# Kernel tuning notes

Measured on AMD Instinct MI355X. Metric: run time of the kernel, lower is better.

The kernel has to match this reference:

```python
import jax, jax.numpy as jnp
import numpy as np


def setup_inputs() -> dict:
    key = jax.random.key(0)
    ks = jax.random.split(key, 8)
    B, C, H, W = 16, 192, 64, 64
    dt_rank, d_state = 12, 1
    return {
        "x": jax.random.normal(ks[0], (B, C, H, W), dtype=jnp.float32),
        "conv_w": jax.random.normal(ks[1], (C, 1, 5, 5), dtype=jnp.float32) * 0.1,
        "conv_b": jax.random.normal(ks[2], (C,), dtype=jnp.float32) * 0.1,
        "x_proj_w": jax.random.normal(ks[3], (dt_rank + 2 * d_state, C), dtype=jnp.float32) * (C ** -0.5),
        "dt_w": jax.random.normal(ks[4], (C, dt_rank), dtype=jnp.float32) * (dt_rank ** -0.5),
        "dt_b": jax.random.normal(ks[5], (C,), dtype=jnp.float32) * 0.1,
        "A_logs": jnp.zeros((C, d_state), dtype=jnp.float32),  # log(arange(1,d_state+1)) with d_state=1 -> 0
        "Ds": jnp.ones((C,), dtype=jnp.float32),
    }


def reference(x, conv_w, conv_b, x_proj_w, dt_w, dt_b, A_logs, Ds):
    B, C, H, W = x.shape
    L = H * W
    dt_rank = dt_w.shape[1]
    n = A_logs.shape[1]  # d_state
    # depthwise conv2d, kernel 5, padding SAME (=d_conv//2), then SiLU
    x = jax.lax.conv_general_dilated(
        x, conv_w, window_strides=(1, 1), padding='SAME',
        feature_group_count=C, dimension_numbers=('NCHW', 'OIHW', 'NCHW'))
    x = jax.nn.silu(x + conv_b[None, :, None, None])
    xs = x.reshape(B, C, L)  # (b, d, l)
    # x_proj: (dt_rank + 2n, C) @ (b, C, l)
    x_dbl = jnp.einsum('kc,bcl->bkl', x_proj_w, xs)
    dts, Bs, Cs = jnp.split(x_dbl, [dt_rank, dt_rank + n], axis=1)
    # dt projection + softplus (delta_softplus=True with delta_bias)
    delta = jax.nn.softplus(jnp.einsum('cr,brl->bcl', dt_w, dts) + dt_b[None, :, None])  # (b,d,l)
    A = -jnp.exp(A_logs)  # (d, n)
    # selective scan returning the full state trajectory h_t (b,d,n,l):
    # h_t = exp(delta_t * A) * h_{t-1} + delta_t * B_t * u_t
    a = jnp.exp(delta[:, :, None, :] * A[None, :, :, None])        # (b,d,n,l)
    b_el = delta[:, :, None, :] * Bs[:, None, :, :] * xs[:, :, None, :]  # (b,d,n,l)

    def combine(e1, e2):
        a1, b1 = e1
        a2, b2 = e2
        return (a1 * a2, a2 * b1 + b2)

    _, h = jax.lax.associative_scan(combine, (a, b_el), axis=-1)  # h: (b,d,n,l)
    state = h.reshape(B, C * n, L)
    # y = C_t * h_t + D * u (fp32, d_state=1 broadcast)
    y = state.astype(jnp.float32) * Cs.astype(jnp.float32) + xs * Ds[:, None]
    return y.reshape(B, C, H, W)
```

## Files before the change

kernel.cpp:

```cpp
#include <hip/hip_runtime.h>
#include <hip/hip_bf16.h>
#include <cstddef>

#define BB 16
#define CC 192
#define HH 64
#define WW 64
#define LL 4096
#define DTR 12
#define KK 14

__device__ __forceinline__ float silu_f(float v) {
  return v / (1.f + __expf(-v));
}

__global__ __launch_bounds__(256) void conv_silu_kernel(
    const float* __restrict__ x, const float* __restrict__ cw,
    const float* __restrict__ cb, float* __restrict__ xs) {
  const int bc = blockIdx.x;
  const int c = bc % CC;
  const int tid = threadIdx.x;
  const int lane = tid & 63;
  const int wv = tid >> 6;
  const int oy0 = wv * 16;

  float w[25];
#pragma unroll
  for (int k = 0; k < 25; ++k) w[k] = cw[c * 25 + k];
  const float bias = cb[c];

  const float* xp = x + (size_t)bc * LL + lane;
  float* op = xs + (size_t)bc * LL + lane;

  float rv[20];
#pragma unroll
  for (int r = 0; r < 20; ++r) {
    const int gr = oy0 + r - 2;
    float v = 0.f;
    if ((unsigned)gr < 64u) v = xp[gr * 64];
    rv[r] = v;
  }

  float acc[5];
#pragma unroll
  for (int i = 0; i < 5; ++i) acc[i] = 0.f;

#pragma unroll
  for (int r = 0; r < 20; ++r) {
    float v = rv[r];
    float vm2 = __shfl_up(v, 2u, 64);
    float vm1 = __shfl_up(v, 1u, 64);
    float vp1 = __shfl_down(v, 1u, 64);
    float vp2 = __shfl_down(v, 2u, 64);
    if (lane < 2) vm2 = 0.f;
    if (lane < 1) vm1 = 0.f;
    if (lane > 62) vp1 = 0.f;
    if (lane > 61) vp2 = 0.f;
    float t[5] = {vm2, vm1, v, vp1, vp2};
#pragma unroll
    for (int ky = 0; ky < 5; ++ky) {
      if (r >= ky && (r - ky) < 16) {
        float s = acc[(r - ky) % 5];
#pragma unroll
        for (int kx = 0; kx < 5; ++kx) s += w[ky * 5 + kx] * t[kx];
        acc[(r - ky) % 5] = s;
      }
    }
    if (r >= 4) {
      const int yf = oy0 + r - 4;
      float a = acc[(r - 4) % 5] + bias;
      op[yf * 64] = silu_f(a);
      acc[(r - 4) % 5] = 0.f;
    }
  }
}

__global__ __launch_bounds__(512) void proj_kernel(
    const float* __restrict__ xs, const float* __restrict__ xpw,
    float* __restrict__ xdbl) {
  const int b = blockIdx.y;
  const int l0 = blockIdx.x * 128;
  const int tid = threadIdx.x;
  const int lane = tid & 63;
  const int g = tid >> 6;

  __shared__ float part[8][KK][132];

  float2 acc[KK];
#pragma unroll
  for (int k = 0; k < KK; ++k) acc[k] = make_float2(0.f, 0.f);

  const float* bp = xs + ((size_t)(b * CC + g * 24)) * LL + l0 + lane * 2;
#pragma unroll 4
  for (int cc = 0; cc < 24; ++cc) {
    float2 v = *(const float2*)(bp + (size_t)cc * LL);
    const int c = g * 24 + cc;
#pragma unroll
    for (int k = 0; k < KK; ++k) {
      float wv = xpw[k * CC + c];
      acc[k].x += wv * v.x;
      acc[k].y += wv * v.y;
    }
  }
#pragma unroll
  for (int k = 0; k < KK; ++k)
    *(float2*)&part[g][k][lane * 2] = acc[k];
  __syncthreads();

  for (int idx = tid; idx < KK * 128; idx += 512) {
    int k = idx >> 7, ln = idx & 127;
    float v = 0.f;
#pragma unroll
    for (int p = 0; p < 8; ++p) v += part[p][k][ln];
    xdbl[((size_t)b * KK + k) * LL + l0 + ln] = v;
  }
}

__global__ __launch_bounds__(64) void scan_kernel(
    const float* __restrict__ xs, const float* __restrict__ xdbl,
    const float* __restrict__ dtw, const float* __restrict__ dtb,
    const float* __restrict__ A_logs, const float* __restrict__ Ds,
    float* __restrict__ y) {
  const int bc = blockIdx.x;
  const int b = bc / CC;
  const int c = bc - b * CC;
  const int lane = threadIdx.x;

  const float Ac = -__expf(A_logs[c]);
  const float Dc = Ds[c];
  float dw[DTR];
#pragma unroll
  for (int r = 0; r < DTR; ++r) dw[r] = dtw[c * DTR + r];
  const float db = dtb[c];

  const float* xp = xs + (size_t)bc * LL;
  const float* xb = xdbl + (size_t)b * KK * LL;
  float* yp = y + (size_t)bc * LL;

  float hcarry = 0.f;

  auto load_chunk = [&](int sc, float4* dst) {
    const int base = sc * 256 + lane * 4;
    dst[0] = *(const float4*)(xp + base);
    dst[1] = *(const float4*)(xb + 12 * LL + base);
    dst[2] = *(const float4*)(xb + 13 * LL + base);
#pragma unroll
    for (int r = 0; r < DTR; ++r)
      dst[3 + r] = *(const float4*)(xb + r * LL + base);
  };

  auto process = [&](int sc, const float4* buf) {
    const int base = sc * 256 + lane * 4;
    const float4 x4 = buf[0];
    const float4 B4 = buf[1];
    const float4 C4 = buf[2];
    float xx[4] = {x4.x, x4.y, x4.z, x4.w};
    float bb[4] = {B4.x, B4.y, B4.z, B4.w};
    float av[4], bv[4];
    float aggA = 1.f, aggB = 0.f;
#pragma unroll
    for (int q = 0; q < 4; ++q) {
      float z = db;
#pragma unroll
      for (int r = 0; r < DTR; ++r) z += dw[r] * ((&buf[3 + r].x)[q]);
      float delta = (z > 15.f) ? z : __logf(1.f + __expf(z));
      float a = __expf(delta * Ac);
      float be = delta * bb[q] * xx[q];
      av[q] = a;
      bv[q] = be;
      aggA = a * aggA;
      aggB = a * aggB + be;
    }

    float incA = aggA, incB = aggB;
#pragma unroll
    for (int s = 1; s < 64; s <<= 1) {
      float pA = __shfl_up(incA, (unsigned)s, 64);
      float pB = __shfl_up(incB, (unsigned)s, 64);
      if (lane >= s) {
        incB = incA * pB + incB;
        incA = incA * pA;
      }
    }
    float eA = __shfl_up(incA, 1u, 64);
    float eB = __shfl_up(incB, 1u, 64);
    if (lane == 0) { eA = 1.f; eB = 0.f; }
    float tA = __shfl(incA, 63, 64);
    float tB = __shfl(incB, 63, 64);

    float h = eA * hcarry + eB;
    float ov[4];
#pragma unroll
    for (int q = 0; q < 4; ++q) {
      h = av[q] * h + bv[q];
      ov[q] = h * ((&C4.x)[q]) + xx[q] * Dc;
    }
    float4 o;
    o.x = ov[0]; o.y = ov[1]; o.z = ov[2]; o.w = ov[3];
    *(float4*)(yp + base) = o;

    hcarry = tA * hcarry + tB;
  };

  float4 bufA[15], bufB[15];
  load_chunk(0, bufA);
  for (int i = 0; i < 8; ++i) {
    const int s0 = 2 * i;
    load_chunk(s0 + 1, bufB);
    process(s0, bufA);
    load_chunk(s0 + 2 < 16 ? s0 + 2 : 15, bufA);
    process(s0 + 1, bufB);
  }
}

extern "C" void kernel_launch(void* const* d_in, const int* in_sizes, int n_in,
                              void* d_out, int out_size, void* d_ws,
                              size_t ws_size, hipStream_t stream) {
  const float* x        = (const float*)d_in[0];
  const float* conv_w   = (const float*)d_in[1];
  const float* conv_b   = (const float*)d_in[2];
  const float* x_proj_w = (const float*)d_in[3];
  const float* dt_w     = (const float*)d_in[4];
  const float* dt_b     = (const float*)d_in[5];
  const float* A_logs   = (const float*)d_in[6];
  const float* Ds       = (const float*)d_in[7];
  float* out = (float*)d_out;

  char* ws = (char*)d_ws;
  const size_t plane_bytes = (size_t)BB * CC * LL * sizeof(float);
  float* xs   = (float*)ws;
  float* xdbl = (float*)(ws + plane_bytes);

  conv_silu_kernel<<<dim3(BB * CC), 256, 0, stream>>>(x, conv_w, conv_b, xs);
  proj_kernel<<<dim3(LL / 128, BB), 512, 0, stream>>>(xs, x_proj_w, xdbl);
  scan_kernel<<<dim3(BB * CC), 64, 0, stream>>>(xs, xdbl, dt_w, dt_b,
                                                A_logs, Ds, out);
}
```

Before: 167.9 us.

## Split scan sequence across four wavefronts with cross-segment carry fixup

The scan kernel now uses 256 threads per (batch, channel) block, and each of its four wavefronts scans a 1024-element segment independently. Each thread keeps per-element cumulative decay products and partial states in registers. Segment summaries are combined through shared memory, and outputs are fixed up with the incoming carry. This removes the serial dependency across 16 chunks within one wavefront and increases parallelism and memory-level concurrency, at the cost of extra registers (u/v arrays), a block barrier, and extra multiplies.

```diff
diff --git a/kernel.cpp b/kernel.cpp
--- a/kernel.cpp
+++ b/kernel.cpp
@@ -116,7 +116,7 @@
   }
 }
 
-__global__ __launch_bounds__(64) void scan_kernel(
+__global__ __launch_bounds__(256) void scan_kernel(
     const float* __restrict__ xs, const float* __restrict__ xdbl,
     const float* __restrict__ dtw, const float* __restrict__ dtb,
     const float* __restrict__ A_logs, const float* __restrict__ Ds,
@@ -124,7 +124,9 @@
   const int bc = blockIdx.x;
   const int b = bc / CC;
   const int c = bc - b * CC;
-  const int lane = threadIdx.x;
+  const int tid = threadIdx.x;
+  const int lane = tid & 63;
+  const int wv = tid >> 6;
 
   const float Ac = -__expf(A_logs[c]);
   const float Dc = Ds[c];
@@ -137,35 +139,34 @@
   const float* xb = xdbl + (size_t)b * KK * LL;
   float* yp = y + (size_t)bc * LL;
 
-  float hcarry = 0.f;
-
-  auto load_chunk = [&](int sc, float4* dst) {
-    const int base = sc * 256 + lane * 4;
-    dst[0] = *(const float4*)(xp + base);
-    dst[1] = *(const float4*)(xb + 12 * LL + base);
-    dst[2] = *(const float4*)(xb + 13 * LL + base);
+  __shared__ float segA[4];
+  __shared__ float segB[4];
+
+  float PA = 1.f;
+  float hB = 0.f;
+  float u[16], v[16];
+
+#pragma unroll
+  for (int ck = 0; ck < 4; ++ck) {
+    const int base = wv * 1024 + ck * 256 + lane * 4;
+    const float4 x4 = *(const float4*)(xp + base);
+    const float4 B4 = *(const float4*)(xb + 12 * LL + base);
+    const float4 C4 = *(const float4*)(xb + 13 * LL + base);
+    float4 dr[DTR];
 #pragma unroll
     for (int r = 0; r < DTR; ++r)
-      dst[3 + r] = *(const float4*)(xb + r * LL + base);
-  };
-
-  auto process = [&](int sc, const float4* buf) {
-    const int base = sc * 256 + lane * 4;
-    const float4 x4 = buf[0];
-    const float4 B4 = buf[1];
-    const float4 C4 = buf[2];
-    float xx[4] = {x4.x, x4.y, x4.z, x4.w};
-    float bb[4] = {B4.x, B4.y, B4.z, B4.w};
+      dr[r] = *(const float4*)(xb + r * LL + base);
+
     float av[4], bv[4];
     float aggA = 1.f, aggB = 0.f;
 #pragma unroll
     for (int q = 0; q < 4; ++q) {
       float z = db;
 #pragma unroll
-      for (int r = 0; r < DTR; ++r) z += dw[r] * ((&buf[3 + r].x)[q]);
+      for (int r = 0; r < DTR; ++r) z += dw[r] * ((&dr[r].x)[q]);
       float delta = (z > 15.f) ? z : __logf(1.f + __expf(z));
       float a = __expf(delta * Ac);
-      float be = delta * bb[q] * xx[q];
+      float be = delta * ((&B4.x)[q]) * ((&x4.x)[q]);
       av[q] = a;
       bv[q] = be;
       aggA = a * aggA;
@@ -185,31 +186,38 @@
     float eA = __shfl_up(incA, 1u, 64);
     float eB = __shfl_up(incB, 1u, 64);
     if (lane == 0) { eA = 1.f; eB = 0.f; }
-    float tA = __shfl(incA, 63, 64);
-    float tB = __shfl(incB, 63, 64);
-
-    float h = eA * hcarry + eB;
-    float ov[4];
+    const float tA = __shfl(incA, 63, 64);
+    const float tB = __shfl(incB, 63, 64);
+
+    float h = eA * hB + eB;
+    float P = PA * eA;
 #pragma unroll
     for (int q = 0; q < 4; ++q) {
       h = av[q] * h + bv[q];
-      ov[q] = h * ((&C4.x)[q]) + xx[q] * Dc;
-    }
+      P = P * av[q];
+      u[ck * 4 + q] = P * ((&C4.x)[q]);
+      v[ck * 4 + q] = h * ((&C4.x)[q]) + ((&x4.x)[q]) * Dc;
+    }
+
+    hB = tA * hB + tB;
+    PA = PA * tA;
+  }
+
+  if (lane == 0) { segA[wv] = PA; segB[wv] = hB; }
+  __syncthreads();
+
+  float carry = 0.f;
+  for (int i = 0; i < wv; ++i) carry = segA[i] * carry + segB[i];
+
+#pragma unroll
+  for (int ck = 0; ck < 4; ++ck) {
+    const int base = wv * 1024 + ck * 256 + lane * 4;
     float4 o;
-    o.x = ov[0]; o.y = ov[1]; o.z = ov[2]; o.w = ov[3];
+    o.x = u[ck * 4 + 0] * carry + v[ck * 4 + 0];
+    o.y = u[ck * 4 + 1] * carry + v[ck * 4 + 1];
+    o.z = u[ck * 4 + 2] * carry + v[ck * 4 + 2];
+    o.w = u[ck * 4 + 3] * carry + v[ck * 4 + 3];
     *(float4*)(yp + base) = o;
-
-    hcarry = tA * hcarry + tB;
-  };
-
-  float4 bufA[15], bufB[15];
-  load_chunk(0, bufA);
-  for (int i = 0; i < 8; ++i) {
-    const int s0 = 2 * i;
-    load_chunk(s0 + 1, bufB);
-    process(s0, bufA);
-    load_chunk(s0 + 2 < 16 ? s0 + 2 : 15, bufA);
-    process(s0 + 1, bufB);
   }
 }
 
@@ -233,6 +241,6 @@
 
   conv_silu_kernel<<<dim3(BB * CC), 256, 0, stream>>>(x, conv_w, conv_b, xs);
   proj_kernel<<<dim3(LL / 128, BB), 512, 0, stream>>>(xs, x_proj_w, xdbl);
-  scan_kernel<<<dim3(BB * CC), 64, 0, stream>>>(xs, xdbl, dt_w, dt_b,
-                                                A_logs, Ds, out);
-}
+  scan_kernel<<<dim3(BB * CC), 256, 0, stream>>>(xs, xdbl, dt_w, dt_b,
+                                                 A_logs, Ds, out);
+}
```

New measurement: 166.4 us. About the same (-0.9%).
